# Optimization experiments

Hardware: AMD Instinct MI355X
Metric: run time of the kernel (lower is better)

The kernel has to match this reference:

```python
import jax, jax.numpy as jnp
import numpy as np


def setup_inputs() -> dict:
    key = jax.random.key(0)
    kq, kk, kw, kv = jax.random.split(key, 4)
    B, T, Dq, Dk, A = 32, 4096, 512, 512, 512
    q = jax.random.normal(kq, (B, Dq), dtype=jnp.float32)
    k = jax.random.normal(kk, (B, T, Dk), dtype=jnp.float32)
    # Dense kernel over concat([q, k]) last dim -> attention_size (TruncatedNormal 0.02)
    W = jax.random.truncated_normal(kw, -2.0, 2.0, (Dq + Dk, A), dtype=jnp.float32) * 0.02
    b = jnp.zeros((A,), dtype=jnp.float32)
    # VarianceScaling(scale=2.0, 'normal') over fan_in=A
    v = jax.random.normal(kv, (A,), dtype=jnp.float32) * jnp.sqrt(2.0 / A)
    return {"q": q, "k": k, "W": W, "b": b, "v": v}


def reference(q, k, W, b, v):
    # Original: tile q over T, concat with k, Dense(tanh), dot with v.
    # Equivalent (same math) without materializing the [B,T,Dq+Dk] concat:
    # split W into Wq (rows for q part) and Wk (rows for k part).
    Dq = q.shape[-1]
    Wq, Wk = W[:Dq], W[Dq:]
    qp = q @ Wq                                  # [B, A]
    kp = jnp.einsum('btd,da->bta', k, Wk)        # [B, T, A]
    out = jnp.tanh(qp[:, None, :] + kp + b)      # [B, T, A]
    score = jnp.einsum('bta,a->bt', out, v)      # [B, T]
    return score
```

## Files before the change

### kernel.cpp

```cpp
#include <hip/hip_runtime.h>
#include <stdint.h>

#define DQ 512
#define DK 512
#define NA 512
#define NBATCH 32
#define M_TOTAL (NBATCH * 4096)

#define BM 128
#define BK 32
#define KITERS (DK / BK)
#define NBLK 256
#define ROUNDS (M_TOTAL / (BM * NBLK))
#define NT (ROUNDS * KITERS)

typedef __attribute__((ext_vector_type(8))) short bf16x8;
typedef __attribute__((ext_vector_type(4))) float f32x4;

__device__ __forceinline__ void gll16(const void* g, void* l) {
  __builtin_amdgcn_global_load_lds(
      (const __attribute__((address_space(1))) uint32_t*)g,
      (__attribute__((address_space(3))) uint32_t*)l, 16, 0, 0);
}

__device__ __forceinline__ uint32_t pack2bf16(float a, float b) {
  uint32_t ua = __float_as_uint(a) + 0x8000u;
  uint32_t ub = __float_as_uint(b) + 0x8000u;
  return __builtin_amdgcn_perm(ub, ua, 0x07060302);
}

__device__ __forceinline__ float fast_tanh(float x) {
  float e = __expf(2.0f * x);
  return 1.0f - 2.0f * __builtin_amdgcn_rcpf(e + 1.0f);
}

__global__ void prep_kernel(const float* __restrict__ W,
                            const float* __restrict__ q,
                            const float* __restrict__ bias,
                            uint16_t* __restrict__ WkTt,
                            float* __restrict__ qpb) {
  const int tid = threadIdx.x;
  if (blockIdx.x < 64) {
    __shared__ uint16_t T[64][65];
    const int d0 = (blockIdx.x & 7) * 64;
    const int a0 = (blockIdx.x >> 3) * 64;
#pragma unroll
    for (int j = 0; j < 16; ++j) {
      int dd = j * 4 + (tid >> 6);
      int aa = tid & 63;
      uint32_t u = __float_as_uint(W[(size_t)(DQ + d0 + dd) * NA + a0 + aa]) + 0x8000u;
      T[dd][aa] = (uint16_t)(u >> 16);
    }
    __syncthreads();
#pragma unroll
    for (int j = 0; j < 8; ++j) {
      int aa = j * 8 + (tid >> 5);
      int n  = a0 + aa;
      int dp = (tid & 31) * 2;
      int d  = d0 + dp;
      uint32_t val = (uint32_t)T[dp][aa] | ((uint32_t)T[dp + 1][aa] << 16);
      *(uint32_t*)(WkTt + (size_t)(d >> 5) * 16384 + n * 32 + (d & 31)) = val;
    }
  } else {
    const int bb = blockIdx.x - 64;
    const int b  = bb >> 1;
    const int a  = (bb & 1) * 256 + tid;
    const float* qr = q + b * DQ;
    float acc = bias[a];
#pragma unroll 8
    for (int d = 0; d < DQ; ++d)
      acc = fmaf(qr[d], W[(size_t)d * NA + a], acc);
    qpb[b * NA + a] = acc;
  }
}

__global__ __launch_bounds__(1024, 4)
void score_kernel(const float* __restrict__ Kmat,
                  const uint16_t* __restrict__ WkTt,
                  const float* __restrict__ qpb,
                  const float* __restrict__ v,
                  float* __restrict__ out) {
  __shared__ __align__(16) uint16_t Bs[3 * NA * BK];
  __shared__ __align__(16) uint16_t As[2 * BM * BK];
  __shared__ float part[8][BM];

  const int tid  = threadIdx.x;
  const int lane = tid & 63;
  const int w    = tid >> 6;
  const int wc   = w & 7;
  const int wr   = w >> 3;
  const int r16  = lane & 15;
  const int quad = lane >> 4;
  const int sw   = quad ^ ((r16 >> 1) & 3);
  const int bid  = blockIdx.x;

  const uint16_t* bconst0;
  const uint16_t* bconst1;
  {
    int s0 = tid;         int n0 = s0 >> 2, k0 = (s0 & 3) ^ ((n0 >> 1) & 3);
    int s1 = 1024 + tid;  int n1 = s1 >> 2, k1 = (s1 & 3) ^ ((n1 >> 1) & 3);
    bconst0 = WkTt + n0 * 32 + k0 * 8;
    bconst1 = WkTt + n1 * 32 + k1 * 8;
  }
  const int bdst0 = (0 * 1024 + w * 64) * 16;
  const int bdst1 = (1 * 1024 + w * 64) * 16;

  const int arow = tid >> 3;
  const int akp  = (tid & 7) * 4;
  const int As_off = arow * 64 + (((akp >> 3) ^ ((arow >> 1) & 3)) * 16) + (akp & 7) * 2;
  const float* ap = Kmat + (size_t)bid * BM * DK + (size_t)arow * DK + akp;

  const int a_ro = (wr * 64 + r16) * 64 + sw * 16;
  const int b_ro = (wc * 64 + r16) * 64 + sw * 16;

  f32x4 acc[4][4];
#pragma unroll
  for (int i = 0; i < 4; ++i)
#pragma unroll
    for (int j = 0; j < 4; ++j) { f32x4 z = {0.f, 0.f, 0.f, 0.f}; acc[i][j] = z; }

  float vv[4];
#pragma unroll
  for (int ns = 0; ns < 4; ++ns) vv[ns] = v[wc * 64 + ns * 16 + r16];

  float4 c = *(const float4*)ap;
  ap += BK;
  gll16((const void*)bconst0, (void*)((char*)Bs + bdst0));
  gll16((const void*)bconst1, (void*)((char*)Bs + bdst1));
  asm volatile("s_waitcnt vmcnt(2)" ::: "memory");
  {
    uint2 p; p.x = pack2bf16(c.x, c.y); p.y = pack2bf16(c.z, c.w);
    *(uint2*)((char*)As + As_off) = p;
  }
  c = *(const float4*)ap;
  ap += BK;
  gll16((const void*)(bconst0 + 16384), (void*)((char*)Bs + 32768 + bdst0));
  gll16((const void*)(bconst1 + 16384), (void*)((char*)Bs + 32768 + bdst1));

  int rdB = 0;
#pragma unroll 1
  for (int t = 0; t < NT; ++t) {
    if (t < NT - 1)
      asm volatile("s_waitcnt vmcnt(2) lgkmcnt(0)" ::: "memory");
    else
      asm volatile("s_waitcnt vmcnt(0) lgkmcnt(0)" ::: "memory");
    __builtin_amdgcn_s_barrier();

    if (t + 1 < NT) {
      uint2 p; p.x = pack2bf16(c.x, c.y); p.y = pack2bf16(c.z, c.w);
      *(uint2*)((char*)As + ((t + 1) & 1) * 8192 + As_off) = p;
    }
    if (t + 2 < NT) {
      c = *(const float4*)ap;
      ap += BK;
      if (((t + 3) & 15) == 0) ap += (size_t)NBLK * BM * DK - DK;
      asm volatile("" ::: "memory");
      int wrB = rdB + 2; if (wrB >= 3) wrB -= 3;
      const int itn = (t + 2) & 15;
      gll16((const void*)(bconst0 + itn * 16384), (void*)((char*)Bs + wrB * 32768 + bdst0));
      gll16((const void*)(bconst1 + itn * 16384), (void*)((char*)Bs + wrB * 32768 + bdst1));
    }

    const char* Abase = (const char*)As + (t & 1) * 8192;
    const char* Bbase = (const char*)Bs + rdB * 32768;
    bf16x8 af[4], bfr[4];
#pragma unroll
    for (int ms = 0; ms < 4; ++ms) af[ms] = *(const bf16x8*)(Abase + a_ro + ms * 1024);
#pragma unroll
    for (int ns = 0; ns < 4; ++ns) bfr[ns] = *(const bf16x8*)(Bbase + b_ro + ns * 1024);
#pragma unroll
    for (int ms = 0; ms < 4; ++ms)
#pragma unroll
      for (int ns = 0; ns < 4; ++ns)
        acc[ms][ns] = __builtin_amdgcn_mfma_f32_16x16x32_bf16(
            af[ms], bfr[ns], acc[ms][ns], 0, 0, 0);

    if ((t & 15) == 15) {
      const int tile  = bid + (t >> 4) * NBLK;
      const int b_idx = tile >> 5;
      float qv[4];
#pragma unroll
      for (int ns = 0; ns < 4; ++ns) qv[ns] = qpb[b_idx * NA + wc * 64 + ns * 16 + r16];
#pragma unroll
      for (int ms = 0; ms < 4; ++ms) {
#pragma unroll
        for (int reg = 0; reg < 4; ++reg) {
          float s = 0.f;
#pragma unroll
          for (int ns = 0; ns < 4; ++ns) {
            float x = acc[ms][ns][reg] + qv[ns];
            s = fmaf(fast_tanh(x), vv[ns], s);
          }
          s += __shfl_xor(s, 1);
          s += __shfl_xor(s, 2);
          s += __shfl_xor(s, 4);
          s += __shfl_xor(s, 8);
          if (r16 == 0) part[wc][wr * 64 + ms * 16 + quad * 4 + reg] = s;
        }
      }
      asm volatile("s_waitcnt lgkmcnt(0)" ::: "memory");
      __builtin_amdgcn_s_barrier();
      if (tid < BM) {
        float s = 0.f;
#pragma unroll
        for (int cg = 0; cg < 8; ++cg) s += part[cg][tid];
        out[(size_t)tile * BM + tid] = s;
      }
#pragma unroll
      for (int i = 0; i < 4; ++i)
#pragma unroll
        for (int j = 0; j < 4; ++j) { f32x4 z = {0.f, 0.f, 0.f, 0.f}; acc[i][j] = z; }
    }
    rdB += 1; if (rdB == 3) rdB = 0;
  }
}

extern "C" void kernel_launch(void* const* d_in, const int* in_sizes, int n_in,
                              void* d_out, int out_size, void* d_ws, size_t ws_size,
                              hipStream_t stream) {
  const float* q = (const float*)d_in[0];
  const float* k = (const float*)d_in[1];
  const float* W = (const float*)d_in[2];
  const float* b = (const float*)d_in[3];
  const float* v = (const float*)d_in[4];
  float* out = (float*)d_out;

  float* qpb = (float*)d_ws;
  uint16_t* WkTt = (uint16_t*)((char*)d_ws + 65536);

  prep_kernel<<<128, 256, 0, stream>>>(W, q, b, WkTt, qpb);
  score_kernel<<<NBLK, 1024, 0, stream>>>(k, WkTt, qpb, v, out);
}
```

Baseline: 434.4 us.

## Halve score-kernel waves with larger per-wave N tile; split qp prep over more blocks

The score kernel drops from 16 to 8 waves per block, and each wave now computes a 64x128 tile (4x8 MFMA accumulators) instead of 64x64. This roughly halves the A-fragment LDS reads per MFMA. Each thread now loads twice as much K and WkT data per step. The prep kernel's q@Wq product is split across 4 segments of the reduction with a shared-memory combine, using 256 blocks instead of 64. The trade-off is more accumulator registers per wave and fewer waves to hide latency.

```diff
diff --git a/kernel.cpp b/kernel.cpp
--- a/kernel.cpp
+++ b/kernel.cpp
@@ -62,19 +62,28 @@
       *(uint32_t*)(WkTt + (size_t)(d >> 5) * 16384 + n * 32 + (d & 31)) = val;
     }
   } else {
-    const int bb = blockIdx.x - 64;
-    const int b  = bb >> 1;
-    const int a  = (bb & 1) * 256 + tid;
-    const float* qr = q + b * DQ;
-    float acc = bias[a];
+    __shared__ float pr[4][64];
+    const int bb  = blockIdx.x - 64;
+    const int b   = bb >> 3;
+    const int a0  = (bb & 7) * 64;
+    const int al  = tid & 63;
+    const int seg = tid >> 6;
+    const float* qr = q + b * DQ + seg * 128;
+    const float* wp = W + (size_t)(seg * 128) * NA + a0 + al;
+    float acc = 0.f;
 #pragma unroll 8
-    for (int d = 0; d < DQ; ++d)
-      acc = fmaf(qr[d], W[(size_t)d * NA + a], acc);
-    qpb[b * NA + a] = acc;
-  }
-}
-
-__global__ __launch_bounds__(1024, 4)
+    for (int i = 0; i < 128; ++i)
+      acc = fmaf(qr[i], wp[(size_t)i * NA], acc);
+    pr[seg][al] = acc;
+    __syncthreads();
+    if (tid < 64) {
+      float s = bias[a0 + tid] + pr[0][tid] + pr[1][tid] + pr[2][tid] + pr[3][tid];
+      qpb[b * NA + a0 + tid] = s;
+    }
+  }
+}
+
+__global__ __launch_bounds__(512, 2)
 void score_kernel(const float* __restrict__ Kmat,
                   const uint16_t* __restrict__ WkTt,
                   const float* __restrict__ qpb,
@@ -82,112 +91,132 @@
                   float* __restrict__ out) {
   __shared__ __align__(16) uint16_t Bs[3 * NA * BK];
   __shared__ __align__(16) uint16_t As[2 * BM * BK];
-  __shared__ float part[8][BM];
+  __shared__ float part[4][BM];
 
   const int tid  = threadIdx.x;
   const int lane = tid & 63;
   const int w    = tid >> 6;
-  const int wc   = w & 7;
-  const int wr   = w >> 3;
+  const int wc   = w & 3;
+  const int wr   = w >> 2;
   const int r16  = lane & 15;
   const int quad = lane >> 4;
   const int sw   = quad ^ ((r16 >> 1) & 3);
   const int bid  = blockIdx.x;
 
-  const uint16_t* bconst0;
-  const uint16_t* bconst1;
+  const uint16_t* bconst[4];
+#pragma unroll
+  for (int j = 0; j < 4; ++j) {
+    int s = j * 512 + tid;
+    int n = s >> 2;
+    int k = (s & 3) ^ ((n >> 1) & 3);
+    bconst[j] = WkTt + n * 32 + k * 8;
+  }
+  const int bdst[4] = { (0 * 512 + w * 64) * 16, (1 * 512 + w * 64) * 16,
+                        (2 * 512 + w * 64) * 16, (3 * 512 + w * 64) * 16 };
+
+  const int arow = tid >> 2;
+  const int qk   = tid & 3;
+  const int rs   = (arow >> 1) & 3;
+  const int ao0  = arow * 64 + (((qk >> 1) ^ rs) * 16) + (qk & 1) * 8;
+  const int ao1  = arow * 64 + (((2 + (qk >> 1)) ^ rs) * 16) + (qk & 1) * 8;
+  const float* ap = Kmat + (size_t)bid * BM * DK + (size_t)arow * DK + qk * 4;
+
+  const int a_ro = (wr * 64 + r16) * 64 + sw * 16;
+  const int b_ro = (wc * 128 + r16) * 64 + sw * 16;
+
+  f32x4 acc[4][8];
+#pragma unroll
+  for (int i = 0; i < 4; ++i)
+#pragma unroll
+    for (int j = 0; j < 8; ++j) { f32x4 z = {0.f, 0.f, 0.f, 0.f}; acc[i][j] = z; }
+
+  float vv[8];
+#pragma unroll
+  for (int ns = 0; ns < 8; ++ns) vv[ns] = v[wc * 128 + ns * 16 + r16];
+
+  float4 c0 = *(const float4*)ap;
+  float4 c1 = *(const float4*)(ap + 16);
+  ap += BK;
+#pragma unroll
+  for (int j = 0; j < 4; ++j)
+    gll16((const void*)bconst[j], (void*)((char*)Bs + bdst[j]));
+  asm volatile("s_waitcnt vmcnt(4)" ::: "memory");
   {
-    int s0 = tid;         int n0 = s0 >> 2, k0 = (s0 & 3) ^ ((n0 >> 1) & 3);
-    int s1 = 1024 + tid;  int n1 = s1 >> 2, k1 = (s1 & 3) ^ ((n1 >> 1) & 3);
-    bconst0 = WkTt + n0 * 32 + k0 * 8;
-    bconst1 = WkTt + n1 * 32 + k1 * 8;
-  }
-  const int bdst0 = (0 * 1024 + w * 64) * 16;
-  const int bdst1 = (1 * 1024 + w * 64) * 16;
-
-  const int arow = tid >> 3;
-  const int akp  = (tid & 7) * 4;
-  const int As_off = arow * 64 + (((akp >> 3) ^ ((arow >> 1) & 3)) * 16) + (akp & 7) * 2;
-  const float* ap = Kmat + (size_t)bid * BM * DK + (size_t)arow * DK + akp;
-
-  const int a_ro = (wr * 64 + r16) * 64 + sw * 16;
-  const int b_ro = (wc * 64 + r16) * 64 + sw * 16;
-
-  f32x4 acc[4][4];
-#pragma unroll
-  for (int i = 0; i < 4; ++i)
-#pragma unroll
-    for (int j = 0; j < 4; ++j) { f32x4 z = {0.f, 0.f, 0.f, 0.f}; acc[i][j] = z; }
-
-  float vv[4];
-#pragma unroll
-  for (int ns = 0; ns < 4; ++ns) vv[ns] = v[wc * 64 + ns * 16 + r16];
-
-  float4 c = *(const float4*)ap;
+    uint2 p0, p1;
+    p0.x = pack2bf16(c0.x, c0.y); p0.y = pack2bf16(c0.z, c0.w);
+    p1.x = pack2bf16(c1.x, c1.y); p1.y = pack2bf16(c1.z, c1.w);
+    *(uint2*)((char*)As + ao0) = p0;
+    *(uint2*)((char*)As + ao1) = p1;
+  }
+  c0 = *(const float4*)ap;
+  c1 = *(const float4*)(ap + 16);
   ap += BK;
-  gll16((const void*)bconst0, (void*)((char*)Bs + bdst0));
-  gll16((const void*)bconst1, (void*)((char*)Bs + bdst1));
-  asm volatile("s_waitcnt vmcnt(2)" ::: "memory");
-  {
-    uint2 p; p.x = pack2bf16(c.x, c.y); p.y = pack2bf16(c.z, c.w);
-    *(uint2*)((char*)As + As_off) = p;
-  }
-  c = *(const float4*)ap;
-  ap += BK;
-  gll16((const void*)(bconst0 + 16384), (void*)((char*)Bs + 32768 + bdst0));
-  gll16((const void*)(bconst1 + 16384), (void*)((char*)Bs + 32768 + bdst1));
+#pragma unroll
+  for (int j = 0; j < 4; ++j)
+    gll16((const void*)(bconst[j] + 16384), (void*)((char*)Bs + 32768 + bdst[j]));
 
   int rdB = 0;
 #pragma unroll 1
   for (int t = 0; t < NT; ++t) {
     if (t < NT - 1)
-      asm volatile("s_waitcnt vmcnt(2) lgkmcnt(0)" ::: "memory");
+      asm volatile("s_waitcnt vmcnt(4) lgkmcnt(0)" ::: "memory");
     else
       asm volatile("s_waitcnt vmcnt(0) lgkmcnt(0)" ::: "memory");
     __builtin_amdgcn_s_barrier();
 
     if (t + 1 < NT) {
-      uint2 p; p.x = pack2bf16(c.x, c.y); p.y = pack2bf16(c.z, c.w);
-      *(uint2*)((char*)As + ((t + 1) & 1) * 8192 + As_off) = p;
+      uint2 p0, p1;
+      p0.x = pack2bf16(c0.x, c0.y); p0.y = pack2bf16(c0.z, c0.w);
+      p1.x = pack2bf16(c1.x, c1.y); p1.y = pack2bf16(c1.z, c1.w);
+      *(uint2*)((char*)As + ((t + 1) & 1) * 8192 + ao0) = p0;
+      *(uint2*)((char*)As + ((t + 1) & 1) * 8192 + ao1) = p1;
     }
     if (t + 2 < NT) {
-      c = *(const float4*)ap;
+      c0 = *(const float4*)ap;
+      c1 = *(const float4*)(ap + 16);
       ap += BK;
       if (((t + 3) & 15) == 0) ap += (size_t)NBLK * BM * DK - DK;
       asm volatile("" ::: "memory");
       int wrB = rdB + 2; if (wrB >= 3) wrB -= 3;
       const int itn = (t + 2) & 15;
-      gll16((const void*)(bconst0 + itn * 16384), (void*)((char*)Bs + wrB * 32768 + bdst0));
-      gll16((const void*)(bconst1 + itn * 16384), (void*)((char*)Bs + wrB * 32768 + bdst1));
+#pragma unroll
+      for (int j = 0; j < 4; ++j)
+        gll16((const void*)(bconst[j] + itn * 16384),
+              (void*)((char*)Bs + wrB * 32768 + bdst[j]));
     }
 
     const char* Abase = (const char*)As + (t & 1) * 8192;
     const char* Bbase = (const char*)Bs + rdB * 32768;
-    bf16x8 af[4], bfr[4];
+    bf16x8 af[4];
 #pragma unroll
     for (int ms = 0; ms < 4; ++ms) af[ms] = *(const bf16x8*)(Abase + a_ro + ms * 1024);
 #pragma unroll
-    for (int ns = 0; ns < 4; ++ns) bfr[ns] = *(const bf16x8*)(Bbase + b_ro + ns * 1024);
-#pragma unroll
-    for (int ms = 0; ms < 4; ++ms)
-#pragma unroll
-      for (int ns = 0; ns < 4; ++ns)
-        acc[ms][ns] = __builtin_amdgcn_mfma_f32_16x16x32_bf16(
-            af[ms], bfr[ns], acc[ms][ns], 0, 0, 0);
+    for (int h = 0; h < 2; ++h) {
+      bf16x8 bh[4];
+#pragma unroll
+      for (int j = 0; j < 4; ++j)
+        bh[j] = *(const bf16x8*)(Bbase + b_ro + (h * 4 + j) * 1024);
+#pragma unroll
+      for (int ms = 0; ms < 4; ++ms)
+#pragma unroll
+        for (int j = 0; j < 4; ++j)
+          acc[ms][h * 4 + j] = __builtin_amdgcn_mfma_f32_16x16x32_bf16(
+              af[ms], bh[j], acc[ms][h * 4 + j], 0, 0, 0);
+    }
 
     if ((t & 15) == 15) {
       const int tile  = bid + (t >> 4) * NBLK;
       const int b_idx = tile >> 5;
-      float qv[4];
-#pragma unroll
-      for (int ns = 0; ns < 4; ++ns) qv[ns] = qpb[b_idx * NA + wc * 64 + ns * 16 + r16];
+      float qv[8];
+#pragma unroll
+      for (int ns = 0; ns < 8; ++ns) qv[ns] = qpb[b_idx * NA + wc * 128 + ns * 16 + r16];
 #pragma unroll
       for (int ms = 0; ms < 4; ++ms) {
 #pragma unroll
         for (int reg = 0; reg < 4; ++reg) {
           float s = 0.f;
 #pragma unroll
-          for (int ns = 0; ns < 4; ++ns) {
+          for (int ns = 0; ns < 8; ++ns) {
             float x = acc[ms][ns][reg] + qv[ns];
             s = fmaf(fast_tanh(x), vv[ns], s);
           }
@@ -201,15 +230,13 @@
       asm volatile("s_waitcnt lgkmcnt(0)" ::: "memory");
       __builtin_amdgcn_s_barrier();
       if (tid < BM) {
-        float s = 0.f;
-#pragma unroll
-        for (int cg = 0; cg < 8; ++cg) s += part[cg][tid];
+        float s = part[0][tid] + part[1][tid] + part[2][tid] + part[3][tid];
         out[(size_t)tile * BM + tid] = s;
       }
 #pragma unroll
       for (int i = 0; i < 4; ++i)
 #pragma unroll
-        for (int j = 0; j < 4; ++j) { f32x4 z = {0.f, 0.f, 0.f, 0.f}; acc[i][j] = z; }
+        for (int j = 0; j < 8; ++j) { f32x4 z = {0.f, 0.f, 0.f, 0.f}; acc[i][j] = z; }
     }
     rdB += 1; if (rdB == 3) rdB = 0;
   }
@@ -228,6 +255,6 @@
   float* qpb = (float*)d_ws;
   uint16_t* WkTt = (uint16_t*)((char*)d_ws + 65536);
 
-  prep_kernel<<<128, 256, 0, stream>>>(W, q, b, WkTt, qpb);
-  score_kernel<<<NBLK, 1024, 0, stream>>>(k, WkTt, qpb, v, out);
-}
+  prep_kernel<<<320, 256, 0, stream>>>(W, q, b, WkTt, qpb);
+  score_kernel<<<NBLK, 512, 0, stream>>>(k, WkTt, qpb, v, out);
+}
```

New measurement: 435.6 us. No clear change (+0.3%).
